# Kernel tuning notes

Measured on AMD Instinct MI355X. Metric: run time of the kernel, lower is better.

## Reference

```python
import jax, jax.numpy as jnp
import numpy as np

B, S, D, H, DK, DV = 4, 2048, 1024, 16, 64, 64
LN_EPS = 1e-5

def setup_inputs() -> dict:
    key = jax.random.key(0)
    ks = jax.random.split(key, 5)
    s = 0.02  # init scale for weights
    return {
        "tokens": jax.random.normal(ks[0], (B, S, D), jnp.float32),
        "Wq": jax.random.normal(ks[1], (H, D, DK), jnp.float32) * s,
        "Wk": jax.random.normal(ks[2], (H, D, DK), jnp.float32) * s,
        "Wv": jax.random.normal(ks[3], (H, D, DV), jnp.float32) * s,
        "Wo": jax.random.normal(ks[4], (H * DV, D), jnp.float32) * s,
        "gamma": jnp.ones((D,), jnp.float32),
        "beta": jnp.zeros((D,), jnp.float32),
    }

def reference(tokens, Wq, Wk, Wv, Wo, gamma, beta):
    # tokens: [B,S,D]; Wq/Wk: [H,D,DK]; Wv: [H,D,DV]; Wo: [H*DV, D]
    d_k = Wq.shape[-1]
    q = jnp.einsum('bsd,hdk->bhsk', tokens, Wq)
    k = jnp.einsum('bsd,hdk->bhsk', tokens, Wk)
    v = jnp.einsum('bsd,hdv->bhsv', tokens, Wv)
    # Faithful quirk of the original: attention() returns (Q K^T / sqrt(d_k)).transpose,
    # so attn[b,h,j,i] = q_i . k_j / sqrt(d_k) and softmax runs over the QUERY index i.
    attn = jnp.einsum('bhik,bhjk->bhji', q, k) / jnp.sqrt(jnp.float32(d_k))
    attn = jax.nn.softmax(attn, axis=-1)
    heads = jnp.einsum('bhji,bhiv->bhjv', attn, v)          # [B,H,S,DV]
    b, s = tokens.shape[0], tokens.shape[1]
    multi = jnp.transpose(heads, (0, 2, 1, 3)).reshape(b, s, -1)  # concat heads
    out = multi @ Wo + tokens                                # out-proj + residual
    mu = jnp.mean(out, axis=-1, keepdims=True)
    var = jnp.var(out, axis=-1, keepdims=True)
    out = (out - mu) / jnp.sqrt(var + LN_EPS) * gamma + beta  # LayerNorm
    return out
```

## Files before the change

kernel.cpp:

```cpp
#include <hip/hip_runtime.h>
#include <hip/hip_bf16.h>
#include <stdint.h>

typedef __attribute__((ext_vector_type(4))) float f32x4;
typedef __attribute__((ext_vector_type(16))) float f32x16;
typedef __attribute__((ext_vector_type(8))) short bf16x8;
typedef __attribute__((ext_vector_type(4))) unsigned short u16x4;
typedef unsigned short u16;
typedef uint32_t u32;

#define B_ 4
#define S_ 2048
#define D_ 1024
#define H_ 16
#define DK_ 64
#define BS_ (B_*S_)
#define NQKV_ (3*H_*DK_)
#define NT_ (S_/64)

#define QSCALE 0.18033688011112042f

__device__ __forceinline__ u16 f2bf(float x) {
  union { float f; uint32_t u; } c; c.f = x;
  uint32_t r = (c.u + 0x7FFFu + ((c.u >> 16) & 1u)) >> 16;
  return (u16)r;
}

__device__ __forceinline__ float exp2_fast(float x) {
  float r; asm("v_exp_f32 %0, %1" : "=v"(r) : "v"(x)); return r;
}

__device__ __forceinline__ void gl_lds16(const u16* g, u16* l) {
  __builtin_amdgcn_global_load_lds(
      (const __attribute__((address_space(1))) u32*)g,
      (__attribute__((address_space(3))) u32*)l, 16, 0, 0);
}

__global__ __launch_bounds__(256) void conv_f32_to_bf16(
    const float* __restrict__ src, u16* __restrict__ dst, int n) {
  int i = (blockIdx.x * 256 + threadIdx.x) * 4;
  if (i >= n) return;
  const float* p = src + i;
  u16x4 o = { f2bf(p[0]), f2bf(p[1]), f2bf(p[2]), f2bf(p[3]) };
  *(u16x4*)(dst + i) = o;
}

__global__ __launch_bounds__(256) void build_wcatT(
    const float* __restrict__ Wq, const float* __restrict__ Wk,
    const float* __restrict__ Wv, u16* __restrict__ dst) {
  __shared__ float Tl[64][65];
  const int slice = blockIdx.y;
  const int w = slice >> 4, hh = slice & 15;
  const int d0 = blockIdx.x * 64;
  const float scale = (w == 0) ? QSCALE : 1.0f;
  const float* src = (w == 0 ? Wq : (w == 1 ? Wk : Wv)) + (long)hh * D_ * DK_;
  {
    int r = threadIdx.x >> 2, c = (threadIdx.x & 3) * 16;
    const float* g = src + (long)(d0 + r) * DK_ + c;
#pragma unroll
    for (int j = 0; j < 16; ++j) Tl[r][c + j] = g[j];
  }
  __syncthreads();
  {
    int dk = threadIdx.x >> 2, c = (threadIdx.x & 3) * 16;
    __attribute__((aligned(16))) u16 tmp[16];
#pragma unroll
    for (int j = 0; j < 16; ++j) tmp[j] = f2bf(Tl[c + j][dk] * scale);
    u16* o = dst + ((long)slice * 64 + dk) * D_ + d0 + c;
    *(bf16x8*)o = *(const bf16x8*)&tmp[0];
    *(bf16x8*)(o + 8) = *(const bf16x8*)&tmp[8];
  }
}

__global__ __launch_bounds__(256) void transpose_f2b(
    const float* __restrict__ src, u16* __restrict__ dst, int R, int C) {
  __shared__ float Tl[64][65];
  const int r0 = blockIdx.y * 64, c0 = blockIdx.x * 64;
  {
    int r = threadIdx.x >> 2, c = (threadIdx.x & 3) * 16;
    const float* g = src + (long)(r0 + r) * C + c0 + c;
#pragma unroll
    for (int j = 0; j < 16; ++j) Tl[r][c + j] = g[j];
  }
  __syncthreads();
  {
    int rr = threadIdx.x >> 2, c = (threadIdx.x & 3) * 16;
    __attribute__((aligned(16))) u16 tmp[16];
#pragma unroll
    for (int j = 0; j < 16; ++j) tmp[j] = f2bf(Tl[c + j][rr]);
    u16* o = dst + (long)(c0 + rr) * R + r0 + c;
    *(bf16x8*)o = *(const bf16x8*)&tmp[0];
    *(bf16x8*)(o + 8) = *(const bf16x8*)&tmp[8];
  }
}

template<bool OUT_BF16, bool VSPLIT>
__global__ __launch_bounds__(256) void gemm_bf16(
    const u16* __restrict__ A, const u16* __restrict__ BT,
    void* __restrict__ Cout, const float* __restrict__ resid,
    u16* __restrict__ vtout, int M, int N, int K) {
  __shared__ __attribute__((aligned(16))) u16 Al[3][128][32];
  __shared__ __attribute__((aligned(16))) u16 Bl[3][128][32];
  const int tid = threadIdx.x;
  const int wid = tid >> 6;
  const int lane = tid & 63;
  const int wm = (wid >> 1) * 64;
  const int wn = (wid & 1) * 64;
  const int row0 = blockIdx.x * 128;
  const int col0 = blockIdx.y * 128;
  const int fr = lane & 15;
  const int g = lane >> 4;

  const int srow = lane >> 2;
  const int sch = lane & 3;

  const int r0a = 32 * wid + srow;
  f32x4 acc[4][4] = {};

#define GSTAGE(bufi, kk)                                                       \
  {                                                                            \
    _Pragma("unroll")                                                          \
    for (int s = 0; s < 2; ++s) {                                              \
      int r = r0a + 16 * s;                                                    \
      int gc = (sch ^ ((r >> 1) & 3)) * 8;                                     \
      gl_lds16(A + (long)(row0 + r) * K + (kk) + gc, &Al[bufi][32 * wid + 16 * s][0]); \
      gl_lds16(BT + (long)(col0 + r) * K + (kk) + gc, &Bl[bufi][32 * wid + 16 * s][0]); \
    }                                                                          \
  }

  const int nt = K >> 5;
  GSTAGE(0, 0);

  for (int t = 0; t < nt; ++t) {
    const int cur = t % 3;
    if (t + 1 < nt) {
      GSTAGE((t + 1) % 3, (t + 1) << 5);
      asm volatile("s_waitcnt vmcnt(4)" ::: "memory");
    } else {
      asm volatile("s_waitcnt vmcnt(0)" ::: "memory");
    }
    __builtin_amdgcn_s_barrier();
    asm volatile("" ::: "memory");

    bf16x8 af[4], bfr[4];
#pragma unroll
    for (int mf = 0; mf < 4; ++mf) {
      int row = wm + mf * 16 + fr;
      af[mf] = *(const bf16x8*)&Al[cur][row][(g ^ ((row >> 1) & 3)) * 8];
    }
#pragma unroll
    for (int nf = 0; nf < 4; ++nf) {
      int row = wn + nf * 16 + fr;
      bfr[nf] = *(const bf16x8*)&Bl[cur][row][(g ^ ((row >> 1) & 3)) * 8];
    }
    __builtin_amdgcn_s_setprio(1);
#pragma unroll
    for (int mf = 0; mf < 4; ++mf)
#pragma unroll
      for (int nf = 0; nf < 4; ++nf)
        acc[mf][nf] = __builtin_amdgcn_mfma_f32_16x16x32_bf16(
            af[mf], bfr[nf], acc[mf][nf], 0, 0, 0);
    __builtin_amdgcn_s_setprio(0);
  }
#undef GSTAGE

  const int r0 = (lane >> 4) * 4;
  if constexpr (VSPLIT) {
    if (col0 >= 2048) {
#pragma unroll
      for (int mf = 0; mf < 4; ++mf)
#pragma unroll
        for (int nf = 0; nf < 4; ++nf) {
          int colv = col0 + wn + nf * 16 + fr - 2048;
          long row = row0 + wm + mf * 16 + r0;
          int b2 = (int)(row >> 11);
          int i = (int)(row & 2047);
          u16x4 o = { f2bf(acc[mf][nf][0]), f2bf(acc[mf][nf][1]),
                      f2bf(acc[mf][nf][2]), f2bf(acc[mf][nf][3]) };
          *(u16x4*)(vtout + ((long)(b2 * 16 + (colv >> 6)) * 64 + (colv & 63)) * S_ + i) = o;
        }
      return;
    }
  }
#pragma unroll
  for (int mf = 0; mf < 4; ++mf)
#pragma unroll
    for (int nf = 0; nf < 4; ++nf)
#pragma unroll
      for (int r = 0; r < 4; ++r) {
        long row = row0 + wm + mf * 16 + r0 + r;
        long col = col0 + wn + nf * 16 + fr;
        if constexpr (OUT_BF16) {
          ((u16*)Cout)[row * N + col] = f2bf(acc[mf][nf][r]);
        } else {
          float v = acc[mf][nf][r] + resid[row * N + col];
          ((float*)Cout)[row * N + col] = v;
        }
      }
}

__global__ __launch_bounds__(512, 4) void attn_kernel(
    const u16* __restrict__ qkv, const u16* __restrict__ vt,
    u16* __restrict__ multi) {
  __shared__ __attribute__((aligned(16))) u16 smem[3][2][64][64];
  const int tid = threadIdx.x;
  const int wid = tid >> 6;
  const int lane = tid & 63;
  const int jl = lane & 31;
  const int h = lane >> 5;

  const int bid = blockIdx.x;
  const int bh = bid & 63;
  const int jt = bid >> 6;
  const int b = bh >> 4, hh = bh & 15;
  const long rowb = (long)b * S_;
  const long rj0 = rowb + (long)jt * 256 + wid * 32;
  const int cbQ = hh * 64, cbK = (H_ + hh) * 64;

#define XF(r) (((r) ^ ((r) >> 3)) & 7)

  bf16x8 kf[4];
  const u16* kbase = qkv + (rj0 + jl) * NQKV_ + cbK + 8 * h;
#pragma unroll
  for (int ks = 0; ks < 4; ++ks) kf[ks] = *(const bf16x8*)(kbase + 16 * ks);

  const int strow = 8 * wid + (lane >> 3);
  const int stoff = ((lane & 7) ^ XF(strow)) * 8;
  const u16* qsrc = qkv + (rowb + strow) * NQKV_ + cbQ + stoff;
  const u16* vsrc = vt + ((long)bh * 64 + strow) * S_ + stoff;

  f32x16 accT[2] = {};
  float l_run = 0.f;

  auto compute = [&](int cur) {
    f32x16 st[2] = {};
    __builtin_amdgcn_s_setprio(1);
#pragma unroll
    for (int mb = 0; mb < 2; ++mb) {
      int row = 32 * mb + jl;
#pragma unroll
      for (int ks = 0; ks < 4; ++ks) {
        bf16x8 qf = *(const bf16x8*)&smem[cur][0][row][((2 * ks + h) ^ XF(row)) * 8];
        st[mb] = __builtin_amdgcn_mfma_f32_32x32x16_bf16(qf, kf[ks], st[mb], 0, 0, 0);
      }
    }
    __builtin_amdgcn_s_setprio(0);

    float ls0 = 0.f, ls1 = 0.f, ls2 = 0.f, ls3 = 0.f;
#pragma unroll
    for (int mb = 0; mb < 2; ++mb)
#pragma unroll
      for (int r = 0; r < 16; r += 4) {
        float p0 = exp2_fast(st[mb][r + 0]);
        float p1 = exp2_fast(st[mb][r + 1]);
        float p2 = exp2_fast(st[mb][r + 2]);
        float p3 = exp2_fast(st[mb][r + 3]);
        st[mb][r + 0] = p0; st[mb][r + 1] = p1;
        st[mb][r + 2] = p2; st[mb][r + 3] = p3;
        ls0 += p0; ls1 += p1; ls2 += p2; ls3 += p3;
      }
    float lsum = (ls0 + ls1) + (ls2 + ls3);
    lsum += __shfl_xor(lsum, 32);
    l_run += lsum;

    uint32_t q32[2][8];
#pragma unroll
    for (int mb = 0; mb < 2; ++mb)
#pragma unroll
      for (int rp = 0; rp < 8; ++rp) {
        __hip_bfloat162 bb = __float22bfloat162_rn(
            make_float2(st[mb][2 * rp], st[mb][2 * rp + 1]));
        uint32_t w; __builtin_memcpy(&w, &bb, 4);
        q32[mb][rp] = w;
      }

    __builtin_amdgcn_s_setprio(1);
#pragma unroll
    for (int ks = 0; ks < 4; ++ks) {
      const int mb = ks >> 1;
      const int A0 = (2 * ks) & 3, A1 = (2 * ks + 1) & 3;
      uint32_t a0 = q32[mb][2 * A0], a1 = q32[mb][2 * A1];
      uint32_t b0 = q32[mb][2 * A0 + 1], b1 = q32[mb][2 * A1 + 1];
      asm("v_permlane32_swap_b32 %0, %1" : "+v"(a0), "+v"(a1));
      asm("v_permlane32_swap_b32 %0, %1" : "+v"(b0), "+v"(b1));
      union { bf16x8 v; uint32_t u[4]; } pa;
      pa.u[0] = a0; pa.u[1] = b0; pa.u[2] = a1; pa.u[3] = b1;
#pragma unroll
      for (int mb2 = 0; mb2 < 2; ++mb2) {
        int row = 32 * mb2 + jl;
        bf16x8 vf = *(const bf16x8*)&smem[cur][1][row][((2 * ks + h) ^ XF(row)) * 8];
        accT[mb2] = __builtin_amdgcn_mfma_f32_32x32x16_bf16(vf, pa.v, accT[mb2], 0, 0, 0);
      }
    }
    __builtin_amdgcn_s_setprio(0);
  };

  gl_lds16(qsrc, &smem[0][0][8 * wid][0]);
  gl_lds16(vsrc, &smem[0][1][8 * wid][0]);
  qsrc += (long)64 * NQKV_; vsrc += 64;

  for (int it = 0; it < NT_ - 1; ++it) {
    const int nx = (it + 1) % 3;
    gl_lds16(qsrc, &smem[nx][0][8 * wid][0]);
    gl_lds16(vsrc, &smem[nx][1][8 * wid][0]);
    qsrc += (long)64 * NQKV_; vsrc += 64;
    asm volatile("s_waitcnt vmcnt(2)" ::: "memory");
    __builtin_amdgcn_s_barrier();
    asm volatile("" ::: "memory");
    compute(it % 3);
  }
  asm volatile("s_waitcnt vmcnt(0)" ::: "memory");
  __builtin_amdgcn_s_barrier();
  asm volatile("" ::: "memory");
  compute((NT_ - 1) % 3);
#undef XF

  __syncthreads();
  u16 (*Wl)[32][72] = (u16 (*)[32][72])&smem[0][0][0][0];
  float inv = 1.f / l_run;
#pragma unroll
  for (int mb2 = 0; mb2 < 2; ++mb2)
#pragma unroll
    for (int r = 0; r < 16; ++r) {
      int d = 32 * mb2 + (r & 3) + 8 * (r >> 2) + 4 * h;
      Wl[wid][jl][d] = f2bf(accT[mb2][r] * inv);
    }
  int j2 = lane >> 1, dh = (lane & 1) * 32;
#pragma unroll
  for (int c = 0; c < 4; ++c) {
    bf16x8 vrow = *(const bf16x8*)&Wl[wid][j2][dh + 8 * c];
    *(bf16x8*)(multi + (rj0 + j2) * (H_ * DK_) + hh * 64 + dh + 8 * c) = vrow;
  }
}

__global__ __launch_bounds__(256) void ln_kernel(
    float* __restrict__ out, const float* __restrict__ gamma,
    const float* __restrict__ beta) {
  const int tid = threadIdx.x;
  const int wid = tid >> 6;
  const int lane = tid & 63;
  float* p = out + (long)blockIdx.x * D_;
  const float* pv = p + tid * 4;
  float x0 = pv[0], x1 = pv[1], x2 = pv[2], x3 = pv[3];
  float s = x0 + x1 + x2 + x3;
  float q = x0 * x0 + x1 * x1 + x2 * x2 + x3 * x3;
#pragma unroll
  for (int off = 32; off > 0; off >>= 1) {
    s += __shfl_down(s, off);
    q += __shfl_down(q, off);
  }
  __shared__ float sh[8];
  if (lane == 0) { sh[wid] = s; sh[4 + wid] = q; }
  __syncthreads();
  s = sh[0] + sh[1] + sh[2] + sh[3];
  q = sh[4] + sh[5] + sh[6] + sh[7];
  float mean = s * (1.0f / D_);
  float var = q * (1.0f / D_) - mean * mean;
  float rstd = rsqrtf(var + 1e-5f);
  const float* g = gamma + tid * 4;
  const float* be = beta + tid * 4;
  float* po = p + tid * 4;
  po[0] = (x0 - mean) * rstd * g[0] + be[0];
  po[1] = (x1 - mean) * rstd * g[1] + be[1];
  po[2] = (x2 - mean) * rstd * g[2] + be[2];
  po[3] = (x3 - mean) * rstd * g[3] + be[3];
}

extern "C" void kernel_launch(void* const* d_in, const int* in_sizes, int n_in,
                              void* d_out, int out_size, void* d_ws, size_t ws_size,
                              hipStream_t stream) {
  const float* tokens = (const float*)d_in[0];
  const float* Wq = (const float*)d_in[1];
  const float* Wk = (const float*)d_in[2];
  const float* Wv = (const float*)d_in[3];
  const float* Wo = (const float*)d_in[4];
  const float* gamma = (const float*)d_in[5];
  const float* beta = (const float*)d_in[6];
  float* out = (float*)d_out;

  char* ws = (char*)d_ws;
  u16* tok_bf = (u16*)(ws);
  u16* wcatT  = (u16*)(ws + 16777216);
  u16* woT    = (u16*)(ws + 23068672);
  u16* qkv    = (u16*)(ws + 25165824);
  u16* multi  = (u16*)(ws + 75497472);
  u16* vt     = (u16*)(ws + 92274688);

  conv_f32_to_bf16<<<8192, 256, 0, stream>>>(tokens, tok_bf, BS_ * D_);
  build_wcatT<<<dim3(16, 48), 256, 0, stream>>>(Wq, Wk, Wv, wcatT);
  transpose_f2b<<<dim3(16, 16), 256, 0, stream>>>(Wo, woT, D_, D_);

  gemm_bf16<true, true><<<dim3(BS_ / 128, NQKV_ / 128), 256, 0, stream>>>(
      tok_bf, wcatT, qkv, nullptr, vt, BS_, NQKV_, D_);

  attn_kernel<<<512, 512, 0, stream>>>(qkv, vt, multi);

  gemm_bf16<false, false><<<dim3(BS_ / 128, D_ / 128), 256, 0, stream>>>(
      multi, woT, out, tokens, nullptr, BS_, D_, D_);

  ln_kernel<<<BS_, 256, 0, stream>>>(out, gamma, beta);
}
```

Before: 198.0 us.

## Merge weight-prep kernels, read bf16 residual, restructure attention per query block

Combines the QKV weight transpose and Wo transpose into a single launch, which removes one kernel launch. The out-projection epilogue now reads the residual from the bf16 token copy instead of the fp32 tokens, halving residual read traffic at the cost of rounding the residual to bf16. The attention inner loop is reorganised to compute, exponentiate and accumulate PV per 32-row query block, lowering live registers for the score tiles. The extra residual precision loss may affect accuracy.

```diff
diff --git a/kernel.cpp b/kernel.cpp
--- a/kernel.cpp
+++ b/kernel.cpp
@@ -26,6 +26,11 @@
   return (u16)r;
 }
 
+__device__ __forceinline__ float bf2f(u16 x) {
+  union { uint32_t u; float f; } c; c.u = ((uint32_t)x) << 16;
+  return c.f;
+}
+
 __device__ __forceinline__ float exp2_fast(float x) {
   float r; asm("v_exp_f32 %0, %1" : "=v"(r) : "v"(x)); return r;
 }
@@ -45,59 +50,58 @@
   *(u16x4*)(dst + i) = o;
 }
 
-__global__ __launch_bounds__(256) void build_wcatT(
+__global__ __launch_bounds__(256) void prep_weights(
     const float* __restrict__ Wq, const float* __restrict__ Wk,
-    const float* __restrict__ Wv, u16* __restrict__ dst) {
+    const float* __restrict__ Wv, const float* __restrict__ Wo,
+    u16* __restrict__ wcatT, u16* __restrict__ woT) {
   __shared__ float Tl[64][65];
-  const int slice = blockIdx.y;
-  const int w = slice >> 4, hh = slice & 15;
-  const int d0 = blockIdx.x * 64;
-  const float scale = (w == 0) ? QSCALE : 1.0f;
-  const float* src = (w == 0 ? Wq : (w == 1 ? Wk : Wv)) + (long)hh * D_ * DK_;
-  {
-    int r = threadIdx.x >> 2, c = (threadIdx.x & 3) * 16;
-    const float* g = src + (long)(d0 + r) * DK_ + c;
-#pragma unroll
-    for (int j = 0; j < 16; ++j) Tl[r][c + j] = g[j];
-  }
-  __syncthreads();
-  {
-    int dk = threadIdx.x >> 2, c = (threadIdx.x & 3) * 16;
-    __attribute__((aligned(16))) u16 tmp[16];
-#pragma unroll
-    for (int j = 0; j < 16; ++j) tmp[j] = f2bf(Tl[c + j][dk] * scale);
-    u16* o = dst + ((long)slice * 64 + dk) * D_ + d0 + c;
-    *(bf16x8*)o = *(const bf16x8*)&tmp[0];
-    *(bf16x8*)(o + 8) = *(const bf16x8*)&tmp[8];
-  }
-}
-
-__global__ __launch_bounds__(256) void transpose_f2b(
-    const float* __restrict__ src, u16* __restrict__ dst, int R, int C) {
-  __shared__ float Tl[64][65];
-  const int r0 = blockIdx.y * 64, c0 = blockIdx.x * 64;
-  {
-    int r = threadIdx.x >> 2, c = (threadIdx.x & 3) * 16;
-    const float* g = src + (long)(r0 + r) * C + c0 + c;
-#pragma unroll
-    for (int j = 0; j < 16; ++j) Tl[r][c + j] = g[j];
-  }
-  __syncthreads();
-  {
-    int rr = threadIdx.x >> 2, c = (threadIdx.x & 3) * 16;
-    __attribute__((aligned(16))) u16 tmp[16];
-#pragma unroll
-    for (int j = 0; j < 16; ++j) tmp[j] = f2bf(Tl[c + j][rr]);
-    u16* o = dst + (long)(c0 + rr) * R + r0 + c;
-    *(bf16x8*)o = *(const bf16x8*)&tmp[0];
-    *(bf16x8*)(o + 8) = *(const bf16x8*)&tmp[8];
+  const int y = blockIdx.y;
+  if (y < 48) {
+    const int w = y >> 4, hh = y & 15;
+    const int d0 = blockIdx.x * 64;
+    const float scale = (w == 0) ? QSCALE : 1.0f;
+    const float* src = (w == 0 ? Wq : (w == 1 ? Wk : Wv)) + (long)hh * D_ * DK_;
+    {
+      int r = threadIdx.x >> 2, c = (threadIdx.x & 3) * 16;
+      const float* g = src + (long)(d0 + r) * DK_ + c;
+#pragma unroll
+      for (int j = 0; j < 16; ++j) Tl[r][c + j] = g[j];
+    }
+    __syncthreads();
+    {
+      int dk = threadIdx.x >> 2, c = (threadIdx.x & 3) * 16;
+      __attribute__((aligned(16))) u16 tmp[16];
+#pragma unroll
+      for (int j = 0; j < 16; ++j) tmp[j] = f2bf(Tl[c + j][dk] * scale);
+      u16* o = wcatT + ((long)y * 64 + dk) * D_ + d0 + c;
+      *(bf16x8*)o = *(const bf16x8*)&tmp[0];
+      *(bf16x8*)(o + 8) = *(const bf16x8*)&tmp[8];
+    }
+  } else {
+    const int r0 = (y - 48) * 64, c0 = blockIdx.x * 64;
+    {
+      int r = threadIdx.x >> 2, c = (threadIdx.x & 3) * 16;
+      const float* g = Wo + (long)(r0 + r) * D_ + c0 + c;
+#pragma unroll
+      for (int j = 0; j < 16; ++j) Tl[r][c + j] = g[j];
+    }
+    __syncthreads();
+    {
+      int rr = threadIdx.x >> 2, c = (threadIdx.x & 3) * 16;
+      __attribute__((aligned(16))) u16 tmp[16];
+#pragma unroll
+      for (int j = 0; j < 16; ++j) tmp[j] = f2bf(Tl[c + j][rr]);
+      u16* o = woT + (long)(c0 + rr) * D_ + r0 + c;
+      *(bf16x8*)o = *(const bf16x8*)&tmp[0];
+      *(bf16x8*)(o + 8) = *(const bf16x8*)&tmp[8];
+    }
   }
 }
 
 template<bool OUT_BF16, bool VSPLIT>
 __global__ __launch_bounds__(256) void gemm_bf16(
     const u16* __restrict__ A, const u16* __restrict__ BT,
-    void* __restrict__ Cout, const float* __restrict__ resid,
+    void* __restrict__ Cout, const u16* __restrict__ resid,
     u16* __restrict__ vtout, int M, int N, int K) {
   __shared__ __attribute__((aligned(16))) u16 Al[3][128][32];
   __shared__ __attribute__((aligned(16))) u16 Bl[3][128][32];
@@ -113,7 +117,6 @@
 
   const int srow = lane >> 2;
   const int sch = lane & 3;
-
   const int r0a = 32 * wid + srow;
   f32x4 acc[4][4] = {};
 
@@ -193,7 +196,7 @@
         if constexpr (OUT_BF16) {
           ((u16*)Cout)[row * N + col] = f2bf(acc[mf][nf][r]);
         } else {
-          float v = acc[mf][nf][r] + resid[row * N + col];
+          float v = acc[mf][nf][r] + bf2f(resid[row * N + col]);
           ((float*)Cout)[row * N + col] = v;
         }
       }
@@ -229,102 +232,81 @@
   const u16* qsrc = qkv + (rowb + strow) * NQKV_ + cbQ + stoff;
   const u16* vsrc = vt + ((long)bh * 64 + strow) * S_ + stoff;
 
-  f32x16 accT[2] = {};
-  float l_run = 0.f;
-
-  auto compute = [&](int cur) {
-    f32x16 st[2] = {};
-    __builtin_amdgcn_s_setprio(1);
-#pragma unroll
-    for (int mb = 0; mb < 2; ++mb) {
-      int row = 32 * mb + jl;
-#pragma unroll
-      for (int ks = 0; ks < 4; ++ks) {
-        bf16x8 qf = *(const bf16x8*)&smem[cur][0][row][((2 * ks + h) ^ XF(row)) * 8];
-        st[mb] = __builtin_amdgcn_mfma_f32_32x32x16_bf16(qf, kf[ks], st[mb], 0, 0, 0);
-      }
-    }
-    __builtin_amdgcn_s_setprio(0);
-
-    float ls0 = 0.f, ls1 = 0.f, ls2 = 0.f, ls3 = 0.f;
-#pragma unroll
-    for (int mb = 0; mb < 2; ++mb)
-#pragma unroll
-      for (int r = 0; r < 16; r += 4) {
-        float p0 = exp2_fast(st[mb][r + 0]);
-        float p1 = exp2_fast(st[mb][r + 1]);
-        float p2 = exp2_fast(st[mb][r + 2]);
-        float p3 = exp2_fast(st[mb][r + 3]);
-        st[mb][r + 0] = p0; st[mb][r + 1] = p1;
-        st[mb][r + 2] = p2; st[mb][r + 3] = p3;
-        ls0 += p0; ls1 += p1; ls2 += p2; ls3 += p3;
-      }
-    float lsum = (ls0 + ls1) + (ls2 + ls3);
-    lsum += __shfl_xor(lsum, 32);
-    l_run += lsum;
-
-    uint32_t q32[2][8];
-#pragma unroll
-    for (int mb = 0; mb < 2; ++mb)
-#pragma unroll
-      for (int rp = 0; rp < 8; ++rp) {
-        __hip_bfloat162 bb = __float22bfloat162_rn(
-            make_float2(st[mb][2 * rp], st[mb][2 * rp + 1]));
-        uint32_t w; __builtin_memcpy(&w, &bb, 4);
-        q32[mb][rp] = w;
-      }
-
-    __builtin_amdgcn_s_setprio(1);
-#pragma unroll
-    for (int ks = 0; ks < 4; ++ks) {
-      const int mb = ks >> 1;
-      const int A0 = (2 * ks) & 3, A1 = (2 * ks + 1) & 3;
-      uint32_t a0 = q32[mb][2 * A0], a1 = q32[mb][2 * A1];
-      uint32_t b0 = q32[mb][2 * A0 + 1], b1 = q32[mb][2 * A1 + 1];
-      asm("v_permlane32_swap_b32 %0, %1" : "+v"(a0), "+v"(a1));
-      asm("v_permlane32_swap_b32 %0, %1" : "+v"(b0), "+v"(b1));
-      union { bf16x8 v; uint32_t u[4]; } pa;
-      pa.u[0] = a0; pa.u[1] = b0; pa.u[2] = a1; pa.u[3] = b1;
-#pragma unroll
-      for (int mb2 = 0; mb2 < 2; ++mb2) {
-        int row = 32 * mb2 + jl;
-        bf16x8 vf = *(const bf16x8*)&smem[cur][1][row][((2 * ks + h) ^ XF(row)) * 8];
-        accT[mb2] = __builtin_amdgcn_mfma_f32_32x32x16_bf16(vf, pa.v, accT[mb2], 0, 0, 0);
-      }
-    }
-    __builtin_amdgcn_s_setprio(0);
-  };
+  f32x16 accT0 = {}, accT1 = {};
+  float l0 = 0.f, l1 = 0.f, l2 = 0.f, l3 = 0.f;
 
   gl_lds16(qsrc, &smem[0][0][8 * wid][0]);
   gl_lds16(vsrc, &smem[0][1][8 * wid][0]);
   qsrc += (long)64 * NQKV_; vsrc += 64;
 
-  for (int it = 0; it < NT_ - 1; ++it) {
-    const int nx = (it + 1) % 3;
-    gl_lds16(qsrc, &smem[nx][0][8 * wid][0]);
-    gl_lds16(vsrc, &smem[nx][1][8 * wid][0]);
-    qsrc += (long)64 * NQKV_; vsrc += 64;
-    asm volatile("s_waitcnt vmcnt(2)" ::: "memory");
+  for (int it = 0; it < NT_; ++it) {
+    const int cur = it % 3;
+    if (it + 1 < NT_) {
+      const int nx = (it + 1) % 3;
+      gl_lds16(qsrc, &smem[nx][0][8 * wid][0]);
+      gl_lds16(vsrc, &smem[nx][1][8 * wid][0]);
+      qsrc += (long)64 * NQKV_; vsrc += 64;
+      asm volatile("s_waitcnt vmcnt(2)" ::: "memory");
+    } else {
+      asm volatile("s_waitcnt vmcnt(0)" ::: "memory");
+    }
     __builtin_amdgcn_s_barrier();
     asm volatile("" ::: "memory");
-    compute(it % 3);
-  }
-  asm volatile("s_waitcnt vmcnt(0)" ::: "memory");
-  __builtin_amdgcn_s_barrier();
-  asm volatile("" ::: "memory");
-  compute((NT_ - 1) % 3);
+
+#pragma unroll
+    for (int mb = 0; mb < 2; ++mb) {
+      const int qrow = 32 * mb + jl;
+      f32x16 st = {};
+      __builtin_amdgcn_s_setprio(1);
+#pragma unroll
+      for (int ks = 0; ks < 4; ++ks) {
+        bf16x8 qf = *(const bf16x8*)&smem[cur][0][qrow][((2 * ks + h) ^ XF(qrow)) * 8];
+        st = __builtin_amdgcn_mfma_f32_32x32x16_bf16(qf, kf[ks], st, 0, 0, 0);
+      }
+      __builtin_amdgcn_s_setprio(0);
+
+      uint32_t q32[8];
+#pragma unroll
+      for (int rp = 0; rp < 8; ++rp) {
+        float p0 = exp2_fast(st[2 * rp]);
+        float p1 = exp2_fast(st[2 * rp + 1]);
+        if (rp & 1) { l2 += p0; l3 += p1; } else { l0 += p0; l1 += p1; }
+        __hip_bfloat162 bb = __float22bfloat162_rn(make_float2(p0, p1));
+        uint32_t w; __builtin_memcpy(&w, &bb, 4);
+        q32[rp] = w;
+      }
+
+      __builtin_amdgcn_s_setprio(1);
+#pragma unroll
+      for (int t2 = 0; t2 < 2; ++t2) {
+        const int ks = 2 * mb + t2;
+        uint32_t a0 = q32[4 * t2 + 0], b0 = q32[4 * t2 + 1];
+        uint32_t a1 = q32[4 * t2 + 2], b1 = q32[4 * t2 + 3];
+        asm("v_permlane32_swap_b32 %0, %1" : "+v"(a0), "+v"(a1));
+        asm("v_permlane32_swap_b32 %0, %1" : "+v"(b0), "+v"(b1));
+        union { bf16x8 v; uint32_t u[4]; } pa;
+        pa.u[0] = a0; pa.u[1] = b0; pa.u[2] = a1; pa.u[3] = b1;
+        bf16x8 vf0 = *(const bf16x8*)&smem[cur][1][jl][((2 * ks + h) ^ XF(jl)) * 8];
+        bf16x8 vf1 = *(const bf16x8*)&smem[cur][1][32 + jl][((2 * ks + h) ^ XF(32 + jl)) * 8];
+        accT0 = __builtin_amdgcn_mfma_f32_32x32x16_bf16(vf0, pa.v, accT0, 0, 0, 0);
+        accT1 = __builtin_amdgcn_mfma_f32_32x32x16_bf16(vf1, pa.v, accT1, 0, 0, 0);
+      }
+      __builtin_amdgcn_s_setprio(0);
+    }
+  }
 #undef XF
 
   __syncthreads();
   u16 (*Wl)[32][72] = (u16 (*)[32][72])&smem[0][0][0][0];
-  float inv = 1.f / l_run;
-#pragma unroll
-  for (int mb2 = 0; mb2 < 2; ++mb2)
-#pragma unroll
-    for (int r = 0; r < 16; ++r) {
-      int d = 32 * mb2 + (r & 3) + 8 * (r >> 2) + 4 * h;
-      Wl[wid][jl][d] = f2bf(accT[mb2][r] * inv);
-    }
+  float lsum = (l0 + l2) + (l1 + l3);
+  lsum += __shfl_xor(lsum, 32);
+  float inv = 1.f / lsum;
+#pragma unroll
+  for (int r = 0; r < 16; ++r) {
+    int d = (r & 3) + 8 * (r >> 2) + 4 * h;
+    Wl[wid][jl][d] = f2bf(accT0[r] * inv);
+    Wl[wid][jl][32 + d] = f2bf(accT1[r] * inv);
+  }
   int j2 = lane >> 1, dh = (lane & 1) * 32;
 #pragma unroll
   for (int c = 0; c < 4; ++c) {
@@ -387,8 +369,7 @@
   u16* vt     = (u16*)(ws + 92274688);
 
   conv_f32_to_bf16<<<8192, 256, 0, stream>>>(tokens, tok_bf, BS_ * D_);
-  build_wcatT<<<dim3(16, 48), 256, 0, stream>>>(Wq, Wk, Wv, wcatT);
-  transpose_f2b<<<dim3(16, 16), 256, 0, stream>>>(Wo, woT, D_, D_);
+  prep_weights<<<dim3(16, 64), 256, 0, stream>>>(Wq, Wk, Wv, Wo, wcatT, woT);
 
   gemm_bf16<true, true><<<dim3(BS_ / 128, NQKV_ / 128), 256, 0, stream>>>(
       tok_bf, wcatT, qkv, nullptr, vt, BS_, NQKV_, D_);
@@ -396,7 +377,7 @@
   attn_kernel<<<512, 512, 0, stream>>>(qkv, vt, multi);
 
   gemm_bf16<false, false><<<dim3(BS_ / 128, D_ / 128), 256, 0, stream>>>(
-      multi, woT, out, tokens, nullptr, BS_, D_, D_);
+      multi, woT, out, tok_bf, nullptr, BS_, D_, D_);
 
   ln_kernel<<<BS_, 256, 0, stream>>>(out, gamma, beta);
 }
```

New measurement: 195.0 us (median of 2 runs). About the same (-1.5%).
